# Performance work log

Measured on AMD Instinct MI355X. Metric: run time of the kernel, lower is better.

## Reference

```python
import jax, jax.numpy as jnp
import numpy as np

N = 100000     # total points
PBS = 500      # point_batch_size (hard-coded in module)
K = 100        # num_neighbors
KP = 15        # num_kernel_points
EPS = 1e-5


def _bn(x, g, b, axes):
    # torch BatchNorm in training mode: batch stats, biased variance
    m = jnp.mean(x, axis=axes, keepdims=True)
    v = jnp.var(x, axis=axes, keepdims=True)
    return (x - m) / jnp.sqrt(v + EPS) * g + b


def setup_inputs() -> dict:
    key = jax.random.key(0)
    ks = jax.random.split(key, 16)
    rn = lambda k, sh, s=1.0: jax.random.normal(k, sh, jnp.float32) * s
    return {
        "pts": rn(ks[0], (N, 3)),
        "normal": rn(ks[1], (N, 3)),
        "kp_points": rn(ks[2], (KP, 3)),
        "kp_weights": rn(ks[3], (KP, 3, 128), 0.3),
        "kp_sigma": jnp.float32(1.0),
        "conv1_w": rn(ks[4], (1024, 128), 128 ** -0.5),
        "conv1_b": rn(ks[5], (1024,), 0.02),
        "bn1_g": jnp.ones((1024,), jnp.float32),
        "bn1_b": jnp.zeros((1024,), jnp.float32),
        "fc1_w": rn(ks[6], (512, 1024), 1024 ** -0.5),
        "fc1_b": rn(ks[7], (512,), 0.02),
        "bn4_g": jnp.ones((512,), jnp.float32),
        "bn4_b": jnp.zeros((512,), jnp.float32),
        "fc2_w": rn(ks[8], (256, 512), 512 ** -0.5),
        "fc2_b": rn(ks[9], (256,), 0.02),
        "bn5_g": jnp.ones((256,), jnp.float32),
        "bn5_b": jnp.zeros((256,), jnp.float32),
        "fc3_w": rn(ks[10], (3, 256), 256 ** -0.5),
        "fc3_b": rn(ks[11], (3,), 0.02),
        "index": jax.random.randint(ks[12], (PBS,), 0, N, jnp.int32),
    }


def reference(pts, normal, kp_points, kp_weights, kp_sigma,
              conv1_w, conv1_b, bn1_g, bn1_b,
              fc1_w, fc1_b, bn4_g, bn4_b,
              fc2_w, fc2_b, bn5_g, bn5_b,
              fc3_w, fc3_b, index):
    sel = pts[index]                                               # [B,3]
    # L-inf pairwise distance and kNN (topk of -dist, as in the torch code)
    dist = jnp.max(jnp.abs(sel[:, None, :] - pts[None, :, :]), axis=-1)  # [B,N]
    _, nbr = jax.lax.top_k(-dist, K)                               # [B,K]
    rel = pts[nbr] - sel[:, None, :]                               # [B,K,3]

    # KPConv: gaussian weights vs kernel points, per-kernel-point linear map
    d2 = jnp.sum((rel[:, :, None, :] - kp_points[None, None]) ** 2, axis=-1)  # [B,K,KP]
    w = jnp.exp(-0.5 * d2 / (kp_sigma ** 2))
    wf = rel[:, :, None, :] * w[..., None]                         # [B,K,KP,3]
    h = jax.nn.relu(jnp.einsum('bnkc,kco->bno', wf, kp_weights))   # [B,K,128]

    # 1x1 conv 128->1024, relu then BN over (batch, points) per channel
    h = jnp.einsum('bnc,oc->bno', h, conv1_w) + conv1_b            # [B,K,1024]
    h = _bn(jax.nn.relu(h), bn1_g, bn1_b, (0, 1))
    feat = jnp.max(h, axis=1)                                      # [B,1024]

    feat = _bn(jax.nn.relu(feat @ fc1_w.T + fc1_b), bn4_g, bn4_b, (0,))
    feat = _bn(jax.nn.relu(feat @ fc2_w.T + fc2_b), bn5_g, bn5_b, (0,))
    feat = feat @ fc3_w.T + fc3_b                                  # [B,3]
    return feat, normal[index]
```

## Files before the change

kernel.cpp:

```cpp
#include <hip/hip_runtime.h>
#include <hip/hip_fp16.h>

#define NPTS 100000
#define NB 500
#define KNN 100
#define KPN 15
#define C1 128
#define C2 1024
#define C3 512
#define C4 256

typedef _Float16 half8 __attribute__((ext_vector_type(8)));
typedef float f32x4 __attribute__((ext_vector_type(4)));

#define QB 2
#define KT 1024
#define CAP 768
#define HS 20
#define HBINS 2048

__device__ __forceinline__ unsigned linf_bits(float px, float py, float pz,
                                              float sx, float sy, float sz) {
  float dx = fabsf(px - sx), dy = fabsf(py - sy), dz = fabsf(pz - sz);
  return __float_as_uint(fmaxf(fmaxf(dx, dy), dz));
}

__global__ __launch_bounds__(KT) void knn_kernel(
    const float* __restrict__ pts, const int* __restrict__ index,
    float* __restrict__ sel, int* __restrict__ nbr) {
  const int b = blockIdx.x;
  const int tid = threadIdx.x;
  __shared__ unsigned hist[QB * HBINS];
  __shared__ unsigned chunk[QB][256];
  __shared__ float qs[QB][3];
  __shared__ int s_kneed[QB], s_cnt[QB], s_shift[QB];
  __shared__ unsigned s_prefix[QB];
  __shared__ int s_direct[QB], s_cnt2[QB];
  __shared__ unsigned cand_bits[QB][CAP];
  __shared__ int cand_idx[QB][CAP];

  for (int j = tid; j < QB * HBINS; j += KT) hist[j] = 0;
  if (tid < QB * 3) {
    int q = tid / 3, c = tid % 3;
    float v = pts[3 * index[b * QB + q] + c];
    qs[q][c] = v;
    sel[(b * QB + q) * 3 + c] = v;
  }
  __syncthreads();
  const float sx0 = qs[0][0], sy0 = qs[0][1], sz0 = qs[0][2];
  const float sx1 = qs[1][0], sy1 = qs[1][1], sz1 = qs[1][2];
  const float4* base4 = (const float4*)pts;

  {
    float4 c6[6], n6[6];
    int i0 = tid * 8;
#pragma unroll
    for (int j = 0; j < 6; ++j) c6[j] = base4[(i0 * 3) / 4 + j];
    for (int it = 0; it < 12; ++it) {
      if (it + 1 < 12) {
        int i1 = (it + 1) * 8192 + tid * 8;
#pragma unroll
        for (int j = 0; j < 6; ++j) n6[j] = base4[(i1 * 3) / 4 + j];
      }
      float px[8], py[8], pz[8];
      px[0] = c6[0].x; py[0] = c6[0].y; pz[0] = c6[0].z;
      px[1] = c6[0].w; py[1] = c6[1].x; pz[1] = c6[1].y;
      px[2] = c6[1].z; py[2] = c6[1].w; pz[2] = c6[2].x;
      px[3] = c6[2].y; py[3] = c6[2].z; pz[3] = c6[2].w;
      px[4] = c6[3].x; py[4] = c6[3].y; pz[4] = c6[3].z;
      px[5] = c6[3].w; py[5] = c6[4].x; pz[5] = c6[4].y;
      px[6] = c6[4].z; py[6] = c6[4].w; pz[6] = c6[5].x;
      px[7] = c6[5].y; py[7] = c6[5].z; pz[7] = c6[5].w;
#pragma unroll
      for (int j = 0; j < 8; ++j) {
        unsigned b0 = linf_bits(px[j], py[j], pz[j], sx0, sy0, sz0);
        unsigned b1 = linf_bits(px[j], py[j], pz[j], sx1, sy1, sz1);
        atomicAdd(&hist[b0 >> HS], 1u);
        atomicAdd(&hist[HBINS + (b1 >> HS)], 1u);
      }
#pragma unroll
      for (int j = 0; j < 6; ++j) c6[j] = n6[j];
    }
    for (int i = 98304 + tid; i < NPTS; i += KT) {
      float px = pts[3 * i], py = pts[3 * i + 1], pz = pts[3 * i + 2];
      atomicAdd(&hist[linf_bits(px, py, pz, sx0, sy0, sz0) >> HS], 1u);
      atomicAdd(&hist[HBINS + (linf_bits(px, py, pz, sx1, sy1, sz1) >> HS)], 1u);
    }
  }
  __syncthreads();

  if (tid < QB * 256) {
    int q = tid >> 8, c = tid & 255;
    unsigned s = 0;
    for (int j = 0; j < 8; ++j) s += hist[q * HBINS + c * 8 + j];
    chunk[q][c] = s;
  }
  __syncthreads();
  if (tid < QB) {
    int q = tid;
    unsigned need = KNN, cum = 0;
    int ch = 0;
    while (ch < 255 && cum + chunk[q][ch] < need) { cum += chunk[q][ch]; ++ch; }
    int bin = ch * 8;
    while (cum + hist[q * HBINS + bin] < need) {
      cum += hist[q * HBINS + bin];
      ++bin;
    }
    s_kneed[q] = (int)(need - cum);
    s_prefix[q] = (unsigned)bin;
    s_cnt[q] = (int)hist[q * HBINS + bin];
    s_shift[q] = HS;
    s_direct[q] = 0;
    s_cnt2[q] = 0;
  }

  for (int q = 0; q < QB; ++q) {
    for (;;) {
      __syncthreads();
      if (s_cnt[q] <= CAP || s_shift[q] == 0) break;
      const int fsh = s_shift[q];
      const unsigned pfx = s_prefix[q];
      const int nsh = (fsh == HS) ? 8 : 0;
      const int nb = (fsh == HS) ? 4096 : 256;
      const float qx = qs[q][0], qy = qs[q][1], qz = qs[q][2];
      for (int j = tid; j < nb; j += KT) hist[j] = 0;
      __syncthreads();
      for (int i = tid; i < NPTS; i += KT) {
        unsigned bits =
            linf_bits(pts[3 * i], pts[3 * i + 1], pts[3 * i + 2], qx, qy, qz);
        if ((bits >> fsh) == pfx) atomicAdd(&hist[(bits >> nsh) & (nb - 1)], 1u);
      }
      __syncthreads();
      if (tid == 0) {
        unsigned need = (unsigned)s_kneed[q], cum = 0;
        int bin = 0;
        while (cum + hist[bin] < need) { cum += hist[bin]; ++bin; }
        s_kneed[q] = (int)(need - cum);
        s_cnt[q] = (int)hist[bin];
        s_prefix[q] = (pfx << ((fsh == HS) ? 12 : 8)) | (unsigned)bin;
        s_shift[q] = nsh;
      }
    }
  }
  __syncthreads();
  const int sh0 = s_shift[0], sh1 = s_shift[1];
  const unsigned pf0 = s_prefix[0], pf1 = s_prefix[1];

  {
    float4 c6[6], n6[6];
    int i0 = tid * 8;
#pragma unroll
    for (int j = 0; j < 6; ++j) c6[j] = base4[(i0 * 3) / 4 + j];
    for (int it = 0; it < 12; ++it) {
      if (it + 1 < 12) {
        int i1 = (it + 1) * 8192 + tid * 8;
#pragma unroll
        for (int j = 0; j < 6; ++j) n6[j] = base4[(i1 * 3) / 4 + j];
      }
      float px[8], py[8], pz[8];
      px[0] = c6[0].x; py[0] = c6[0].y; pz[0] = c6[0].z;
      px[1] = c6[0].w; py[1] = c6[1].x; pz[1] = c6[1].y;
      px[2] = c6[1].z; py[2] = c6[1].w; pz[2] = c6[2].x;
      px[3] = c6[2].y; py[3] = c6[2].z; pz[3] = c6[2].w;
      px[4] = c6[3].x; py[4] = c6[3].y; pz[4] = c6[3].z;
      px[5] = c6[3].w; py[5] = c6[4].x; pz[5] = c6[4].y;
      px[6] = c6[4].z; py[6] = c6[4].w; pz[6] = c6[5].x;
      px[7] = c6[5].y; py[7] = c6[5].z; pz[7] = c6[5].w;
      int ibase = it * 8192 + tid * 8;
#pragma unroll
      for (int j = 0; j < 8; ++j) {
        unsigned b0 = linf_bits(px[j], py[j], pz[j], sx0, sy0, sz0);
        unsigned b1 = linf_bits(px[j], py[j], pz[j], sx1, sy1, sz1);
        unsigned v0 = b0 >> sh0, v1 = b1 >> sh1;
        if (v0 < pf0) {
          int pos = atomicAdd(&s_direct[0], 1);
          nbr[(b * QB + 0) * KNN + pos] = ibase + j;
        } else if (v0 == pf0) {
          int e = atomicAdd(&s_cnt2[0], 1);
          if (e < CAP) { cand_bits[0][e] = b0; cand_idx[0][e] = ibase + j; }
        }
        if (v1 < pf1) {
          int pos = atomicAdd(&s_direct[1], 1);
          nbr[(b * QB + 1) * KNN + pos] = ibase + j;
        } else if (v1 == pf1) {
          int e = atomicAdd(&s_cnt2[1], 1);
          if (e < CAP) { cand_bits[1][e] = b1; cand_idx[1][e] = ibase + j; }
        }
      }
#pragma unroll
      for (int j = 0; j < 6; ++j) c6[j] = n6[j];
    }
    for (int i = 98304 + tid; i < NPTS; i += KT) {
      float px = pts[3 * i], py = pts[3 * i + 1], pz = pts[3 * i + 2];
      unsigned b0 = linf_bits(px, py, pz, sx0, sy0, sz0);
      unsigned b1 = linf_bits(px, py, pz, sx1, sy1, sz1);
      unsigned v0 = b0 >> sh0, v1 = b1 >> sh1;
      if (v0 < pf0) {
        int pos = atomicAdd(&s_direct[0], 1);
        nbr[(b * QB + 0) * KNN + pos] = i;
      } else if (v0 == pf0) {
        int e = atomicAdd(&s_cnt2[0], 1);
        if (e < CAP) { cand_bits[0][e] = b0; cand_idx[0][e] = i; }
      }
      if (v1 < pf1) {
        int pos = atomicAdd(&s_direct[1], 1);
        nbr[(b * QB + 1) * KNN + pos] = i;
      } else if (v1 == pf1) {
        int e = atomicAdd(&s_cnt2[1], 1);
        if (e < CAP) { cand_bits[1][e] = b1; cand_idx[1][e] = i; }
      }
    }
  }
  __syncthreads();

  for (int q = 0; q < QB; ++q) {
    int m = s_cnt2[q] < CAP ? s_cnt2[q] : CAP;
    int base = s_direct[q];
    int kneedq = s_kneed[q];
    for (int c = tid; c < m; c += KT) {
      unsigned bc = cand_bits[q][c];
      int ic = cand_idx[q][c];
      int rank = 0;
      for (int j = 0; j < m; ++j) {
        unsigned bj = cand_bits[q][j];
        rank += (bj < bc || (bj == bc && cand_idx[q][j] < ic)) ? 1 : 0;
      }
      if (rank < kneedq) nbr[(b * QB + q) * KNN + base + rank] = ic;
    }
  }
}

__global__ __launch_bounds__(256) void convert_kernel(
    const float* __restrict__ w1, const float* __restrict__ kpw,
    const float* __restrict__ normal, const int* __restrict__ index,
    __half* __restrict__ wh, __half* __restrict__ kpwT_hi,
    __half* __restrict__ kpwT_lo, float* __restrict__ out2) {
  int i = blockIdx.x * 256 + threadIdx.x;
  if (i < C2 * C1) wh[i] = __float2half(w1[i]);
  if (i < 128 * 64) {
    int o = i >> 6, j = i & 63;
    float v = (j < 45) ? kpw[j * 128 + o] : 0.f;
    __half hi = __float2half_rn(v);
    kpwT_hi[i] = hi;
    kpwT_lo[i] = __float2half_rn(v - __half2float(hi));
  }
  if (i < NB * 3) {
    int b = i / 3, c = i % 3;
    out2[i] = normal[3 * index[b] + c];
  }
}

__global__ __launch_bounds__(256) void kpconv_mfma_kernel(
    const float* __restrict__ pts, const float* __restrict__ sel,
    const int* __restrict__ nbr, const float* __restrict__ kp_points,
    const __half* __restrict__ kpwT_hi, const __half* __restrict__ kpwT_lo,
    const float* __restrict__ kp_sigma, __half* __restrict__ h) {
  const int b = blockIdx.x;
  const int tid = threadIdx.x;
  const int wave = tid >> 6, lane = tid & 63;
  const int lr = lane & 15, quad = lane >> 4;
  __shared__ __half As_hi[112 * 72];
  __shared__ __half As_lo[112 * 72];
  __shared__ __half Bs_hi[128 * 72];
  __shared__ __half Bs_lo[128 * 72];
  __shared__ float rel[100][4];
  __shared__ float kpp[48];

  for (int i = tid; i < 128 * 8; i += 256) {
    int row = i >> 3, seg = i & 7;
    *(float4*)&Bs_hi[row * 72 + seg * 8] =
        *(const float4*)&kpwT_hi[row * 64 + seg * 8];
    *(float4*)&Bs_lo[row * 72 + seg * 8] =
        *(const float4*)&kpwT_lo[row * 64 + seg * 8];
  }
  {
    float4 z = make_float4(0.f, 0.f, 0.f, 0.f);
    for (int i = tid; i < 112 * 8; i += 256) {
      int row = i >> 3, seg = i & 7;
      *(float4*)&As_hi[row * 72 + seg * 8] = z;
      *(float4*)&As_lo[row * 72 + seg * 8] = z;
    }
  }
  if (tid < 45) kpp[tid] = kp_points[tid];
  if (tid < 100) {
    int idx = nbr[b * KNN + tid];
    rel[tid][0] = pts[3 * idx + 0] - sel[b * 3 + 0];
    rel[tid][1] = pts[3 * idx + 1] - sel[b * 3 + 1];
    rel[tid][2] = pts[3 * idx + 2] - sel[b * 3 + 2];
  }
  __syncthreads();

  const float sg = kp_sigma[0];
  const float inv2s2 = -0.5f / (sg * sg);
  for (int i = tid; i < 100 * KPN; i += 256) {
    int k = i / KPN, p = i - k * KPN;
    float rx = rel[k][0] - kpp[p * 3 + 0];
    float ry = rel[k][1] - kpp[p * 3 + 1];
    float rz = rel[k][2] - kpp[p * 3 + 2];
    float w = expf(inv2s2 * (rx * rx + ry * ry + rz * rz));
#pragma unroll
    for (int c = 0; c < 3; ++c) {
      float a = rel[k][c] * w;
      __half hi = __float2half_rn(a);
      As_hi[k * 72 + p * 3 + c] = hi;
      As_lo[k * 72 + p * 3 + c] = __float2half_rn(a - __half2float(hi));
    }
  }
  __syncthreads();

  f32x4 acc[2][7];
#pragma unroll
  for (int t = 0; t < 2; ++t)
#pragma unroll
    for (int m = 0; m < 7; ++m) acc[t][m] = (f32x4)(0.f);

#pragma unroll
  for (int s = 0; s < 2; ++s) {
    half8 bhi[2], blo[2];
#pragma unroll
    for (int t = 0; t < 2; ++t) {
      int boff = ((wave * 2 + t) * 16 + lr) * 72 + s * 32 + quad * 8;
      bhi[t] = *(const half8*)&Bs_hi[boff];
      blo[t] = *(const half8*)&Bs_lo[boff];
    }
#pragma unroll
    for (int m = 0; m < 7; ++m) {
      int aoff = (m * 16 + lr) * 72 + s * 32 + quad * 8;
      half8 ahi = *(const half8*)&As_hi[aoff];
      half8 alo = *(const half8*)&As_lo[aoff];
#pragma unroll
      for (int t = 0; t < 2; ++t) {
        acc[t][m] = __builtin_amdgcn_mfma_f32_16x16x32_f16(ahi, bhi[t],
                                                           acc[t][m], 0, 0, 0);
        acc[t][m] = __builtin_amdgcn_mfma_f32_16x16x32_f16(ahi, blo[t],
                                                           acc[t][m], 0, 0, 0);
        acc[t][m] = __builtin_amdgcn_mfma_f32_16x16x32_f16(alo, bhi[t],
                                                           acc[t][m], 0, 0, 0);
      }
    }
  }

#pragma unroll
  for (int t = 0; t < 2; ++t) {
    int col = (wave * 2 + t) * 16 + lr;
#pragma unroll
    for (int m = 0; m < 7; ++m)
#pragma unroll
      for (int r = 0; r < 4; ++r) {
        int row = m * 16 + quad * 4 + r;
        if (row < 100)
          h[(b * KNN + row) * 128 + col] =
              __float2half_rn(fmaxf(acc[t][m][r], 0.f));
      }
  }
}

__global__ __launch_bounds__(256) void conv1_mfma_kernel(
    const __half* __restrict__ h16, const __half* __restrict__ wh,
    const float* __restrict__ bias, float* __restrict__ featmax,
    float* __restrict__ featmin, float* __restrict__ bnsum,
    float* __restrict__ bnsq) {
  const int b = blockIdx.y;
  const int n0 = blockIdx.x * 128;
  const int tid = threadIdx.x;
  const int wave = tid >> 6, lane = tid & 63;
  const int lr = lane & 15, quad = lane >> 4;
  __shared__ __half Hs[112 * 136];
  __shared__ __half Ws[128 * 136];

  for (int i = tid; i < 112 * 16; i += 256) {
    int row = i >> 4, seg = i & 15;
    float4 v = make_float4(0.f, 0.f, 0.f, 0.f);
    if (row < 100) v = *(const float4*)&h16[(b * 100 + row) * 128 + seg * 8];
    *(float4*)&Hs[row * 136 + seg * 8] = v;
  }
  for (int i = tid; i < 128 * 16; i += 256) {
    int row = i >> 4, seg = i & 15;
    *(float4*)&Ws[row * 136 + seg * 8] =
        *(const float4*)&wh[(n0 + row) * 128 + seg * 8];
  }
  __syncthreads();

  f32x4 acc[2][7];
#pragma unroll
  for (int t = 0; t < 2; ++t)
#pragma unroll
    for (int m = 0; m < 7; ++m) acc[t][m] = (f32x4)(0.f);

#pragma unroll
  for (int s = 0; s < 4; ++s) {
    half8 bfrag[2];
#pragma unroll
    for (int t = 0; t < 2; ++t)
      bfrag[t] =
          *(const half8*)&Ws[((wave * 2 + t) * 16 + lr) * 136 + s * 32 + quad * 8];
#pragma unroll
    for (int m = 0; m < 7; ++m) {
      half8 afrag = *(const half8*)&Hs[(m * 16 + lr) * 136 + s * 32 + quad * 8];
      acc[0][m] =
          __builtin_amdgcn_mfma_f32_16x16x32_f16(afrag, bfrag[0], acc[0][m], 0, 0, 0);
      acc[1][m] =
          __builtin_amdgcn_mfma_f32_16x16x32_f16(afrag, bfrag[1], acc[1][m], 0, 0, 0);
    }
  }

#pragma unroll
  for (int t = 0; t < 2; ++t) {
    int col = n0 + (wave * 2 + t) * 16 + lr;
    float bv = bias[col];
    float pmax = -1e30f, pmin = 1e30f, psum = 0.f, psq = 0.f;
#pragma unroll
    for (int m = 0; m < 7; ++m)
#pragma unroll
      for (int r = 0; r < 4; ++r) {
        int row = m * 16 + quad * 4 + r;
        if (row < 100) {
          float y = fmaxf(acc[t][m][r] + bv, 0.f);
          pmax = fmaxf(pmax, y);
          pmin = fminf(pmin, y);
          psum += y;
          psq += y * y;
        }
      }
    pmax = fmaxf(pmax, __shfl_xor(pmax, 16));
    pmax = fmaxf(pmax, __shfl_xor(pmax, 32));
    pmin = fminf(pmin, __shfl_xor(pmin, 16));
    pmin = fminf(pmin, __shfl_xor(pmin, 32));
    psum += __shfl_xor(psum, 16);
    psum += __shfl_xor(psum, 32);
    psq += __shfl_xor(psq, 16);
    psq += __shfl_xor(psq, 32);
    if (quad == 0) {
      featmax[b * C2 + col] = pmax;
      featmin[b * C2 + col] = pmin;
      atomicAdd(&bnsum[col], psum);
      atomicAdd(&bnsq[col], psq);
    }
  }
}

template <int KDIM, int MODE>
__global__ __launch_bounds__(256) void fc_bn_relu_stats_kernel(
    const float* __restrict__ x1, const float* __restrict__ x2,
    const float* __restrict__ sstat, const float* __restrict__ sqstat,
    const float* __restrict__ bng, const float* __restrict__ bnb,
    const float* __restrict__ w, const float* __restrict__ bias,
    float* __restrict__ yraw, float* __restrict__ s, float* __restrict__ sq,
    int ncols) {
  const int r0 = blockIdx.x * 4;
  const int n0 = blockIdx.y * 64;
  const int tid = threadIdx.x;
  const int col = tid >> 2;
  const int row = tid & 3;
  __shared__ float xs[4][KDIM + 4];
  __shared__ float ws[64][132];
  __shared__ float ao[KDIM], off[KDIM];
  const float invn = (MODE == 1) ? (1.f / (float)(NB * KNN)) : (1.f / (float)NB);
  for (int k = tid; k < KDIM; k += 256) {
    float m = sstat[k] * invn;
    float v = sqstat[k] * invn - m * m;
    float a = bng[k] / sqrtf(v + 1e-5f);
    ao[k] = a;
    off[k] = bnb[k] - m * a;
  }
  __syncthreads();
  for (int f = tid; f < KDIM; f += 256) {
    int rr = f / (KDIM / 4), kq = (f % (KDIM / 4)) * 4;
    float4 xm = *(const float4*)&x1[(r0 + rr) * KDIM + kq];
    float v1[4] = {xm.x, xm.y, xm.z, xm.w};
    if constexpr (MODE == 1) {
      float4 xn = *(const float4*)&x2[(r0 + rr) * KDIM + kq];
      float v2[4] = {xn.x, xn.y, xn.z, xn.w};
#pragma unroll
      for (int j = 0; j < 4; ++j) {
        float a = ao[kq + j];
        float x = (a >= 0.f) ? v1[j] : v2[j];
        xs[rr][kq + j] = x * a + off[kq + j];
      }
    } else {
#pragma unroll
      for (int j = 0; j < 4; ++j)
        xs[rr][kq + j] = v1[j] * ao[kq + j] + off[kq + j];
    }
  }
  float acc = 0.f;
  for (int kc = 0; kc < KDIM; kc += 128) {
    __syncthreads();
#pragma unroll
    for (int i = 0; i < 8; ++i) {
      int f = tid + i * 256;
      int cr = f >> 5, kq = (f & 31) * 4;
      *(float4*)&ws[cr][kq] = *(const float4*)&w[(n0 + cr) * KDIM + kc + kq];
    }
    __syncthreads();
    for (int kk = 0; kk < 128; kk += 4) {
      float4 xv = *(float4*)&xs[row][kc + kk];
      float4 wv = *(float4*)&ws[col][kk];
      acc += xv.x * wv.x + xv.y * wv.y + xv.z * wv.z + xv.w * wv.w;
    }
  }
  float y = fmaxf(acc + bias[n0 + col], 0.f);
  yraw[(r0 + row) * ncols + n0 + col] = y;
  float ys = y, y2 = y * y;
  ys += __shfl_xor(ys, 1); y2 += __shfl_xor(y2, 1);
  ys += __shfl_xor(ys, 2); y2 += __shfl_xor(y2, 2);
  if (row == 0) {
    atomicAdd(&s[n0 + col], ys);
    atomicAdd(&sq[n0 + col], y2);
  }
}

__global__ __launch_bounds__(256) void fc3_bn_kernel(
    const float* __restrict__ f3raw, const float* __restrict__ s5,
    const float* __restrict__ sq5, const float* __restrict__ g5,
    const float* __restrict__ b5, const float* __restrict__ w,
    const float* __restrict__ bias, float* __restrict__ out) {
  __shared__ float ao[C4], off[C4];
  int tid = threadIdx.x;
  {
    float m = s5[tid] * (1.f / (float)NB);
    float v = sq5[tid] * (1.f / (float)NB) - m * m;
    float a = g5[tid] / sqrtf(v + 1e-5f);
    ao[tid] = a;
    off[tid] = b5[tid] - m * a;
  }
  __syncthreads();
  int idx = blockIdx.x * 256 + tid;
  if (idx >= NB * 3) return;
  int b = idx / 3, o = idx % 3;
  float acc = 0.f;
  for (int k = 0; k < C4; ++k)
    acc += (f3raw[b * C4 + k] * ao[k] + off[k]) * w[o * C4 + k];
  out[idx] = acc + bias[o];
}

extern "C" void kernel_launch(void* const* d_in, const int* in_sizes, int n_in,
                              void* d_out, int out_size, void* d_ws,
                              size_t ws_size, hipStream_t stream) {
  const float* pts = (const float*)d_in[0];
  const float* normal = (const float*)d_in[1];
  const float* kp_points = (const float*)d_in[2];
  const float* kp_weights = (const float*)d_in[3];
  const float* kp_sigma = (const float*)d_in[4];
  const float* conv1_w = (const float*)d_in[5];
  const float* conv1_b = (const float*)d_in[6];
  const float* bn1_g = (const float*)d_in[7];
  const float* bn1_b = (const float*)d_in[8];
  const float* fc1_w = (const float*)d_in[9];
  const float* fc1_b = (const float*)d_in[10];
  const float* bn4_g = (const float*)d_in[11];
  const float* bn4_b = (const float*)d_in[12];
  const float* fc2_w = (const float*)d_in[13];
  const float* fc2_b = (const float*)d_in[14];
  const float* bn5_g = (const float*)d_in[15];
  const float* bn5_b = (const float*)d_in[16];
  const float* fc3_w = (const float*)d_in[17];
  const float* fc3_b = (const float*)d_in[18];
  const int* index = (const int*)d_in[19];
  float* out = (float*)d_out;

  char* p = (char*)d_ws;
  auto carve = [&](size_t bytes) {
    void* r = (void*)p;
    p += (bytes + 255) & ~(size_t)255;
    return r;
  };
  float* sel = (float*)carve(NB * 3 * 4);
  int* nbr = (int*)carve(NB * KNN * 4);
  __half* h = (__half*)carve((size_t)NB * KNN * C1 * 2);
  __half* wh = (__half*)carve((size_t)C2 * C1 * 2);
  __half* kpwT_hi = (__half*)carve((size_t)128 * 64 * 2);
  __half* kpwT_lo = (__half*)carve((size_t)128 * 64 * 2);
  float* featmax = (float*)carve(NB * C2 * 4);
  float* featmin = (float*)carve(NB * C2 * 4);
  float* f2raw = (float*)carve(NB * C3 * 4);
  float* f3raw = (float*)carve(NB * C4 * 4);
  float* stats = (float*)carve((2 * C2 + 2 * C3 + 2 * C4) * 4);
  float* bnsum = stats;
  float* bnsq = stats + C2;
  float* s4 = stats + 2 * C2;
  float* sq4 = s4 + C3;
  float* s5 = sq4 + C3;
  float* sq5 = s5 + C4;

  hipMemsetAsync(stats, 0, (2 * C2 + 2 * C3 + 2 * C4) * 4, stream);

  knn_kernel<<<NB / QB, KT, 0, stream>>>(pts, index, sel, nbr);
  convert_kernel<<<(C2 * C1 + 255) / 256, 256, 0, stream>>>(
      conv1_w, kp_weights, normal, index, wh, kpwT_hi, kpwT_lo, out + NB * 3);
  kpconv_mfma_kernel<<<NB, 256, 0, stream>>>(pts, sel, nbr, kp_points, kpwT_hi,
                                             kpwT_lo, kp_sigma, h);
  conv1_mfma_kernel<<<dim3(8, NB), 256, 0, stream>>>(h, wh, conv1_b, featmax,
                                                     featmin, bnsum, bnsq);
  fc_bn_relu_stats_kernel<C2, 1><<<dim3(125, C3 / 64), 256, 0, stream>>>(
      featmax, featmin, bnsum, bnsq, bn1_g, bn1_b, fc1_w, fc1_b, f2raw, s4,
      sq4, C3);
  fc_bn_relu_stats_kernel<C3, 2><<<dim3(125, C4 / 64), 256, 0, stream>>>(
      f2raw, nullptr, s4, sq4, bn4_g, bn4_b, fc2_w, fc2_b, f3raw, s5, sq5, C4);
  fc3_bn_kernel<<<(NB * 3 + 255) / 256, 256, 0, stream>>>(
      f3raw, s5, sq5, bn5_g, bn5_b, fc3_w, fc3_b, out);
}
```

Measured before the change: 317.3 us.

## Replace histogram kNN select with sampled-threshold single-pass candidate filtering

The kNN kernel now handles one query per block. It estimates a distance threshold from a 4096-point sample using radix select, then does a single pass over all points to collect candidates under that threshold, followed by a rank sort. This replaces the full histogram pass plus collection pass and cuts global atomics. If the candidate count falls outside the capacity range, a bounded retry loop repeats the full pass with a new sample rank.

Result: slower. 429.8 us (+35.4%).

```diff
diff --git a/kernel.cpp b/kernel.cpp
--- a/kernel.cpp
+++ b/kernel.cpp
@@ -13,11 +13,9 @@
 typedef _Float16 half8 __attribute__((ext_vector_type(8)));
 typedef float f32x4 __attribute__((ext_vector_type(4)));
 
-#define QB 2
 #define KT 1024
-#define CAP 768
-#define HS 20
-#define HBINS 2048
+#define CAP 2048
+#define SAMP 4096
 
 __device__ __forceinline__ unsigned linf_bits(float px, float py, float pz,
                                               float sx, float sy, float sz) {
@@ -30,203 +28,134 @@
     float* __restrict__ sel, int* __restrict__ nbr) {
   const int b = blockIdx.x;
   const int tid = threadIdx.x;
-  __shared__ unsigned hist[QB * HBINS];
-  __shared__ unsigned chunk[QB][256];
-  __shared__ float qs[QB][3];
-  __shared__ int s_kneed[QB], s_cnt[QB], s_shift[QB];
-  __shared__ unsigned s_prefix[QB];
-  __shared__ int s_direct[QB], s_cnt2[QB];
-  __shared__ unsigned cand_bits[QB][CAP];
-  __shared__ int cand_idx[QB][CAP];
-
-  for (int j = tid; j < QB * HBINS; j += KT) hist[j] = 0;
-  if (tid < QB * 3) {
-    int q = tid / 3, c = tid % 3;
-    float v = pts[3 * index[b * QB + q] + c];
-    qs[q][c] = v;
-    sel[(b * QB + q) * 3 + c] = v;
-  }
-  __syncthreads();
-  const float sx0 = qs[0][0], sy0 = qs[0][1], sz0 = qs[0][2];
-  const float sx1 = qs[1][0], sy1 = qs[1][1], sz1 = qs[1][2];
+  __shared__ unsigned samp[SAMP];
+  __shared__ unsigned hist[256];
+  __shared__ unsigned s_pfx;
+  __shared__ int s_need;
+  __shared__ int s_cnt2;
+  __shared__ unsigned cand_bits[CAP];
+  __shared__ int cand_idx[CAP];
+  __shared__ float qs[3];
+
+  if (tid < 3) {
+    float v = pts[3 * index[b] + tid];
+    qs[tid] = v;
+    sel[b * 3 + tid] = v;
+  }
+  __syncthreads();
+  const float sx = qs[0], sy = qs[1], sz = qs[2];
   const float4* base4 = (const float4*)pts;
 
-  {
-    float4 c6[6], n6[6];
-    int i0 = tid * 8;
-#pragma unroll
-    for (int j = 0; j < 6; ++j) c6[j] = base4[(i0 * 3) / 4 + j];
-    for (int it = 0; it < 12; ++it) {
-      if (it + 1 < 12) {
-        int i1 = (it + 1) * 8192 + tid * 8;
-#pragma unroll
-        for (int j = 0; j < 6; ++j) n6[j] = base4[(i1 * 3) / 4 + j];
-      }
-      float px[8], py[8], pz[8];
-      px[0] = c6[0].x; py[0] = c6[0].y; pz[0] = c6[0].z;
-      px[1] = c6[0].w; py[1] = c6[1].x; pz[1] = c6[1].y;
-      px[2] = c6[1].z; py[2] = c6[1].w; pz[2] = c6[2].x;
-      px[3] = c6[2].y; py[3] = c6[2].z; pz[3] = c6[2].w;
-      px[4] = c6[3].x; py[4] = c6[3].y; pz[4] = c6[3].z;
-      px[5] = c6[3].w; py[5] = c6[4].x; pz[5] = c6[4].y;
-      px[6] = c6[4].z; py[6] = c6[4].w; pz[6] = c6[5].x;
-      px[7] = c6[5].y; py[7] = c6[5].z; pz[7] = c6[5].w;
-#pragma unroll
-      for (int j = 0; j < 8; ++j) {
-        unsigned b0 = linf_bits(px[j], py[j], pz[j], sx0, sy0, sz0);
-        unsigned b1 = linf_bits(px[j], py[j], pz[j], sx1, sy1, sz1);
-        atomicAdd(&hist[b0 >> HS], 1u);
-        atomicAdd(&hist[HBINS + (b1 >> HS)], 1u);
-      }
-#pragma unroll
-      for (int j = 0; j < 6; ++j) c6[j] = n6[j];
-    }
-    for (int i = 98304 + tid; i < NPTS; i += KT) {
-      float px = pts[3 * i], py = pts[3 * i + 1], pz = pts[3 * i + 2];
-      atomicAdd(&hist[linf_bits(px, py, pz, sx0, sy0, sz0) >> HS], 1u);
-      atomicAdd(&hist[HBINS + (linf_bits(px, py, pz, sx1, sy1, sz1) >> HS)], 1u);
-    }
-  }
-  __syncthreads();
-
-  if (tid < QB * 256) {
-    int q = tid >> 8, c = tid & 255;
-    unsigned s = 0;
-    for (int j = 0; j < 8; ++j) s += hist[q * HBINS + c * 8 + j];
-    chunk[q][c] = s;
-  }
-  __syncthreads();
-  if (tid < QB) {
-    int q = tid;
-    unsigned need = KNN, cum = 0;
-    int ch = 0;
-    while (ch < 255 && cum + chunk[q][ch] < need) { cum += chunk[q][ch]; ++ch; }
-    int bin = ch * 8;
-    while (cum + hist[q * HBINS + bin] < need) {
-      cum += hist[q * HBINS + bin];
-      ++bin;
-    }
-    s_kneed[q] = (int)(need - cum);
-    s_prefix[q] = (unsigned)bin;
-    s_cnt[q] = (int)hist[q * HBINS + bin];
-    s_shift[q] = HS;
-    s_direct[q] = 0;
-    s_cnt2[q] = 0;
-  }
-
-  for (int q = 0; q < QB; ++q) {
-    for (;;) {
+#pragma unroll
+  for (int j = 0; j < 4; ++j) {
+    int si = tid * 4 + j;
+    int i = si * 24;
+    samp[si] = linf_bits(pts[3 * i], pts[3 * i + 1], pts[3 * i + 2], sx, sy, sz);
+  }
+  __syncthreads();
+
+  int s = 16, slo = 1, shi = SAMP;
+  int m = 0;
+  for (int attempt = 0; attempt < 12; ++attempt) {
+    unsigned pfx = 0;
+    int need = s;
+    for (int pass = 0; pass < 4; ++pass) {
+      const int sh = 24 - 8 * pass;
+      if (tid < 256) hist[tid] = 0;
       __syncthreads();
-      if (s_cnt[q] <= CAP || s_shift[q] == 0) break;
-      const int fsh = s_shift[q];
-      const unsigned pfx = s_prefix[q];
-      const int nsh = (fsh == HS) ? 8 : 0;
-      const int nb = (fsh == HS) ? 4096 : 256;
-      const float qx = qs[q][0], qy = qs[q][1], qz = qs[q][2];
-      for (int j = tid; j < nb; j += KT) hist[j] = 0;
-      __syncthreads();
-      for (int i = tid; i < NPTS; i += KT) {
-        unsigned bits =
-            linf_bits(pts[3 * i], pts[3 * i + 1], pts[3 * i + 2], qx, qy, qz);
-        if ((bits >> fsh) == pfx) atomicAdd(&hist[(bits >> nsh) & (nb - 1)], 1u);
+      for (int j = tid; j < SAMP; j += KT) {
+        unsigned v = samp[j];
+        bool ok = (pass == 0) || ((v >> (sh + 8)) == pfx);
+        if (ok) atomicAdd(&hist[(v >> sh) & 255u], 1u);
       }
       __syncthreads();
       if (tid == 0) {
-        unsigned need = (unsigned)s_kneed[q], cum = 0;
+        unsigned cum = 0;
         int bin = 0;
-        while (cum + hist[bin] < need) { cum += hist[bin]; ++bin; }
-        s_kneed[q] = (int)(need - cum);
-        s_cnt[q] = (int)hist[bin];
-        s_prefix[q] = (pfx << ((fsh == HS) ? 12 : 8)) | (unsigned)bin;
-        s_shift[q] = nsh;
-      }
-    }
-  }
-  __syncthreads();
-  const int sh0 = s_shift[0], sh1 = s_shift[1];
-  const unsigned pf0 = s_prefix[0], pf1 = s_prefix[1];
-
-  {
-    float4 c6[6], n6[6];
-    int i0 = tid * 8;
-#pragma unroll
-    for (int j = 0; j < 6; ++j) c6[j] = base4[(i0 * 3) / 4 + j];
-    for (int it = 0; it < 12; ++it) {
-      if (it + 1 < 12) {
-        int i1 = (it + 1) * 8192 + tid * 8;
-#pragma unroll
-        for (int j = 0; j < 6; ++j) n6[j] = base4[(i1 * 3) / 4 + j];
-      }
-      float px[8], py[8], pz[8];
-      px[0] = c6[0].x; py[0] = c6[0].y; pz[0] = c6[0].z;
-      px[1] = c6[0].w; py[1] = c6[1].x; pz[1] = c6[1].y;
-      px[2] = c6[1].z; py[2] = c6[1].w; pz[2] = c6[2].x;
-      px[3] = c6[2].y; py[3] = c6[2].z; pz[3] = c6[2].w;
-      px[4] = c6[3].x; py[4] = c6[3].y; pz[4] = c6[3].z;
-      px[5] = c6[3].w; py[5] = c6[4].x; pz[5] = c6[4].y;
-      px[6] = c6[4].z; py[6] = c6[4].w; pz[6] = c6[5].x;
-      px[7] = c6[5].y; py[7] = c6[5].z; pz[7] = c6[5].w;
-      int ibase = it * 8192 + tid * 8;
-#pragma unroll
-      for (int j = 0; j < 8; ++j) {
-        unsigned b0 = linf_bits(px[j], py[j], pz[j], sx0, sy0, sz0);
-        unsigned b1 = linf_bits(px[j], py[j], pz[j], sx1, sy1, sz1);
-        unsigned v0 = b0 >> sh0, v1 = b1 >> sh1;
-        if (v0 < pf0) {
-          int pos = atomicAdd(&s_direct[0], 1);
-          nbr[(b * QB + 0) * KNN + pos] = ibase + j;
-        } else if (v0 == pf0) {
-          int e = atomicAdd(&s_cnt2[0], 1);
-          if (e < CAP) { cand_bits[0][e] = b0; cand_idx[0][e] = ibase + j; }
+        while ((int)(cum + hist[bin]) < need) { cum += hist[bin]; ++bin; }
+        s_pfx = (pfx << 8) | (unsigned)bin;
+        s_need = need - (int)cum;
+      }
+      __syncthreads();
+      pfx = s_pfx;
+      need = s_need;
+    }
+    const unsigned T = pfx;
+
+    if (tid == 0) s_cnt2 = 0;
+    __syncthreads();
+
+    {
+      float4 c6[6], n6[6];
+#pragma unroll
+      for (int j = 0; j < 6; ++j) c6[j] = base4[tid * 6 + j];
+      for (int it = 0; it < 12; ++it) {
+        if (it + 1 < 12) {
+#pragma unroll
+          for (int j = 0; j < 6; ++j)
+            n6[j] = base4[(it + 1) * 6144 + tid * 6 + j];
         }
-        if (v1 < pf1) {
-          int pos = atomicAdd(&s_direct[1], 1);
-          nbr[(b * QB + 1) * KNN + pos] = ibase + j;
-        } else if (v1 == pf1) {
-          int e = atomicAdd(&s_cnt2[1], 1);
-          if (e < CAP) { cand_bits[1][e] = b1; cand_idx[1][e] = ibase + j; }
+        float px[8], py[8], pz[8];
+        px[0] = c6[0].x; py[0] = c6[0].y; pz[0] = c6[0].z;
+        px[1] = c6[0].w; py[1] = c6[1].x; pz[1] = c6[1].y;
+        px[2] = c6[1].z; py[2] = c6[1].w; pz[2] = c6[2].x;
+        px[3] = c6[2].y; py[3] = c6[2].z; pz[3] = c6[2].w;
+        px[4] = c6[3].x; py[4] = c6[3].y; pz[4] = c6[3].z;
+        px[5] = c6[3].w; py[5] = c6[4].x; pz[5] = c6[4].y;
+        px[6] = c6[4].z; py[6] = c6[4].w; pz[6] = c6[5].x;
+        px[7] = c6[5].y; py[7] = c6[5].z; pz[7] = c6[5].w;
+        int ibase = it * 8192 + tid * 8;
+#pragma unroll
+        for (int j = 0; j < 8; ++j) {
+          unsigned bits = linf_bits(px[j], py[j], pz[j], sx, sy, sz);
+          if (bits <= T) {
+            int e = atomicAdd(&s_cnt2, 1);
+            if (e < CAP) {
+              cand_bits[e] = bits;
+              cand_idx[e] = ibase + j;
+            }
+          }
         }
-      }
-#pragma unroll
-      for (int j = 0; j < 6; ++j) c6[j] = n6[j];
-    }
-    for (int i = 98304 + tid; i < NPTS; i += KT) {
-      float px = pts[3 * i], py = pts[3 * i + 1], pz = pts[3 * i + 2];
-      unsigned b0 = linf_bits(px, py, pz, sx0, sy0, sz0);
-      unsigned b1 = linf_bits(px, py, pz, sx1, sy1, sz1);
-      unsigned v0 = b0 >> sh0, v1 = b1 >> sh1;
-      if (v0 < pf0) {
-        int pos = atomicAdd(&s_direct[0], 1);
-        nbr[(b * QB + 0) * KNN + pos] = i;
-      } else if (v0 == pf0) {
-        int e = atomicAdd(&s_cnt2[0], 1);
-        if (e < CAP) { cand_bits[0][e] = b0; cand_idx[0][e] = i; }
-      }
-      if (v1 < pf1) {
-        int pos = atomicAdd(&s_direct[1], 1);
-        nbr[(b * QB + 1) * KNN + pos] = i;
-      } else if (v1 == pf1) {
-        int e = atomicAdd(&s_cnt2[1], 1);
-        if (e < CAP) { cand_bits[1][e] = b1; cand_idx[1][e] = i; }
-      }
-    }
-  }
-  __syncthreads();
-
-  for (int q = 0; q < QB; ++q) {
-    int m = s_cnt2[q] < CAP ? s_cnt2[q] : CAP;
-    int base = s_direct[q];
-    int kneedq = s_kneed[q];
-    for (int c = tid; c < m; c += KT) {
-      unsigned bc = cand_bits[q][c];
-      int ic = cand_idx[q][c];
-      int rank = 0;
-      for (int j = 0; j < m; ++j) {
-        unsigned bj = cand_bits[q][j];
-        rank += (bj < bc || (bj == bc && cand_idx[q][j] < ic)) ? 1 : 0;
-      }
-      if (rank < kneedq) nbr[(b * QB + q) * KNN + base + rank] = ic;
-    }
+#pragma unroll
+        for (int j = 0; j < 6; ++j) c6[j] = n6[j];
+      }
+      for (int i = 98304 + tid; i < NPTS; i += KT) {
+        unsigned bits =
+            linf_bits(pts[3 * i], pts[3 * i + 1], pts[3 * i + 2], sx, sy, sz);
+        if (bits <= T) {
+          int e = atomicAdd(&s_cnt2, 1);
+          if (e < CAP) {
+            cand_bits[e] = bits;
+            cand_idx[e] = i;
+          }
+        }
+      }
+    }
+    __syncthreads();
+    int cnt = s_cnt2;
+    if (cnt >= KNN && cnt <= CAP) {
+      m = cnt;
+      break;
+    }
+    if (cnt < KNN) {
+      slo = s;
+      s = (s * 2 <= shi) ? s * 2 : shi;
+    } else {
+      shi = s;
+      s = (s / 2 >= slo) ? s / 2 : slo;
+    }
+    __syncthreads();
+  }
+
+  for (int c = tid; c < m; c += KT) {
+    unsigned bc = cand_bits[c];
+    int ic = cand_idx[c];
+    int rank = 0;
+    for (int j = 0; j < m; ++j) {
+      unsigned bj = cand_bits[j];
+      rank += (bj < bc || (bj == bc && cand_idx[j] < ic)) ? 1 : 0;
+    }
+    if (rank < KNN) nbr[b * KNN + rank] = ic;
   }
 }
 
@@ -585,7 +514,7 @@
 
   hipMemsetAsync(stats, 0, (2 * C2 + 2 * C3 + 2 * C4) * 4, stream);
 
-  knn_kernel<<<NB / QB, KT, 0, stream>>>(pts, index, sel, nbr);
+  knn_kernel<<<NB, KT, 0, stream>>>(pts, index, sel, nbr);
   convert_kernel<<<(C2 * C1 + 255) / 256, 256, 0, stream>>>(
       conv1_w, kp_weights, normal, index, wh, kpwT_hi, kpwT_lo, out + NB * 3);
   kpconv_mfma_kernel<<<NB, 256, 0, stream>>>(pts, sel, nbr, kp_points, kpwT_hi,
```
